# Kernel optimization log

Hardware: AMD Instinct MI355X
Metric: run time of the kernel (lower is better)

## Reference

```python
import jax, jax.numpy as jnp
import numpy as np

LAYERS = 2          # init kwarg 'layers'
DEPTH = 4           # init kwarg 'depth' (StronglyEntanglingLayers depth)
N_QUBITS = 4
MULT = float(np.pi - np.finfo(np.float32).eps)


def _apply_1q(state, U, q):
    """state: (B,2,2,2,2) complex; U: (2,2) or (B,2,2) complex; wire q (axis 1+q, MSB-first)."""
    st = jnp.moveaxis(state, 1 + q, -1)
    if U.ndim == 3:
        st = jnp.einsum('bij,b...j->b...i', U, st)
    else:
        st = jnp.einsum('ij,...j->...i', U, st)
    return jnp.moveaxis(st, -1, 1 + q)


def _apply_cnot(state, c, t):
    st = jnp.moveaxis(state, (1 + c, 1 + t), (-2, -1))
    st = jnp.stack([st[..., 0, :], st[..., 1, ::-1]], axis=-2)
    return jnp.moveaxis(st, (-2, -1), (1 + c, 1 + t))


def _ry(theta):
    """RY(theta) -> (...,2,2) complex64; theta may be batched."""
    c = jnp.cos(theta / 2).astype(jnp.complex64)
    s = jnp.sin(theta / 2).astype(jnp.complex64)
    return jnp.stack([jnp.stack([c, -s], -1), jnp.stack([s, c], -1)], -2)


def _rot(phi, theta, omega):
    """qml.Rot = RZ(omega) RY(theta) RZ(phi), scalar params -> (2,2) complex64."""
    c = jnp.cos(theta / 2)
    s = jnp.sin(theta / 2)
    ep = jnp.exp(-0.5j * (phi + omega).astype(jnp.complex64))
    em = jnp.exp(0.5j * (phi - omega).astype(jnp.complex64))
    row0 = jnp.stack([ep * c, -em * s])
    row1 = jnp.stack([jnp.conj(em) * s, jnp.conj(ep) * c])
    return jnp.stack([row0, row1])


def _circuit(x, w, n_out):
    """AngleEmbedding(Y) + StronglyEntanglingLayers on 4 qubits.
    x: (B,4) angles; w: (L,4,3); returns (B, n_out) PauliZ expvals."""
    B = x.shape[0]
    state = jnp.zeros((B, 16), jnp.complex64).at[:, 0].set(1.0).reshape(B, 2, 2, 2, 2)
    for q in range(N_QUBITS):
        state = _apply_1q(state, _ry(x[:, q]), q)  # batched RY embedding
    L = w.shape[0]
    for l in range(L):
        for q in range(N_QUBITS):
            state = _apply_1q(state, _rot(w[l, q, 0], w[l, q, 1], w[l, q, 2]), q)
        r = (l % (N_QUBITS - 1)) + 1  # default SEL ranges: 1,2,3,1,...
        for q in range(N_QUBITS):
            state = _apply_cnot(state, q, (q + r) % N_QUBITS)
    probs = state.real ** 2 + state.imag ** 2  # (B,2,2,2,2)
    outs = []
    for q in range(n_out):
        axes = tuple(a for a in range(1, 5) if a != 1 + q)
        pq = probs.sum(axes)  # (B,2)
        outs.append(pq[:, 0] - pq[:, 1])
    return jnp.stack(outs, axis=1)


def _forward(x_, theta):
    B = x_.shape[0]
    z = jnp.zeros((B, 1), x_.dtype)
    H = jnp.concatenate([z, x_, z, z], axis=1)  # (B,16)
    c44 = jax.vmap(lambda xb, wb: _circuit(xb, wb, 4))  # over 4 blocks
    c41 = jax.vmap(lambda xb, wb: _circuit(xb, wb, 1))
    # layer 0: 'first' -> contiguous 4-wide blocks
    blocks = H.reshape(B, 4, 4).transpose(1, 0, 2)  # (block, B, 4)
    H = c44(blocks, theta[0]).transpose(1, 0, 2).reshape(B, 16)
    # hidden layers: 'multiple' -> block j = column j of each old block
    for i in range(LAYERS):
        blocks = H.reshape(B, 4, 4).transpose(2, 0, 1)  # (j, B, old_block)
        H = c44(blocks, theta[i + 3]).transpose(1, 0, 2).reshape(B, 16)
    # 16 -> 4 : 'multiple' transpose, 4to1 readout per block
    blocks = H.reshape(B, 4, 4).transpose(2, 0, 1)
    H = c41(blocks, theta[1]).transpose(1, 0, 2).reshape(B, 4)
    # 4 -> 1 : single block, only theta[2][0] is used (matches original loop)
    H = _circuit(H, theta[2, 0], 1)  # (B,1)
    return (H * MULT).astype(jnp.float32)


def setup_inputs() -> dict:
    key = jax.random.key(0)
    k1, k2 = jax.random.split(key)
    x_ = jax.random.uniform(k1, (32768, 13), dtype=jnp.float32)
    theta = 0.01 * jax.random.normal(k2, (LAYERS + 3, 4, DEPTH, 4, 3), dtype=jnp.float32)
    return {"x_": x_, "theta": theta}


def reference(x_, theta):
    return _forward(x_, theta)
```

## Files before the change

kernel.cpp:

```cpp
#include <hip/hip_runtime.h>
#include <math.h>


typedef _Float16 half8 __attribute__((ext_vector_type(8)));
typedef float floatx16 __attribute__((ext_vector_type(16)));

#define N_CIRC 17
__device__ __constant__ constexpr int PERM[3][16] = {
  {0, 9, 11, 2, 15, 6, 4, 13, 7, 14, 12, 5, 8, 1, 3, 10},
  {0, 5, 10, 15, 1, 4, 11, 14, 2, 7, 8, 13, 3, 6, 9, 12},
  {0, 3, 6, 5, 12, 15, 10, 9, 11, 8, 13, 14, 7, 4, 1, 2},
};

__global__ void __launch_bounds__(64) build_M_kernel(
    const float* __restrict__ theta, _Float16* __restrict__ M) {
  int idx = blockIdx.x * 64 + threadIdx.x;
  if (idx >= N_CIRC * 16) return;
  int c = idx >> 4, j = idx & 15;
  int tt, blk;
  if (c < 4)       { tt = 0; blk = c; }
  else if (c < 8)  { tt = 3; blk = c - 4; }
  else if (c < 12) { tt = 4; blk = c - 8; }
  else if (c < 16) { tt = 1; blk = c - 12; }
  else             { tt = 2; blk = 0; }
  float sr[16], si[16];
#pragma unroll
  for (int i = 0; i < 16; ++i) { sr[i] = 0.f; si[i] = 0.f; }
  sr[j] = 1.f;
#pragma unroll
  for (int l = 0; l < 4; ++l) {
#pragma unroll
    for (int q = 0; q < 4; ++q) {
      const float* th = theta + (((tt * 4 + blk) * 16) + l * 4 + q) * 3;
      float phi = th[0], the = th[1], ome = th[2];
      float st, ct;   __sincosf(0.5f * the, &st, &ct);
      float sap, cap; __sincosf(0.5f * (phi + ome), &sap, &cap);
      float sam, cam; __sincosf(0.5f * (phi - ome), &sam, &cam);
      float u00r =  cap * ct, u00i = -sap * ct;
      float u01r = -cam * st, u01i = -sam * st;
      float u10r =  cam * st, u10i = -sam * st;
      float u11r =  cap * ct, u11i =  sap * ct;
      const int m = 8 >> q;
#pragma unroll
      for (int i = 0; i < 16; ++i) {
        if (i & m) continue;
        const int i1 = i | m;
        float ar = sr[i], ai = si[i], br = sr[i1], bi = si[i1];
        sr[i]  = u00r * ar - u00i * ai + u01r * br - u01i * bi;
        si[i]  = u00r * ai + u00i * ar + u01r * bi + u01i * br;
        sr[i1] = u10r * ar - u10i * ai + u11r * br - u11i * bi;
        si[i1] = u10r * ai + u10i * ar + u11r * bi + u11i * br;
      }
    }
    const int ri = (l == 3) ? 0 : l;
    float tr[16], ti[16];
#pragma unroll
    for (int i = 0; i < 16; ++i) { tr[i] = sr[i]; ti[i] = si[i]; }
#pragma unroll
    for (int i = 0; i < 16; ++i) { sr[PERM[ri][i]] = tr[i]; si[PERM[ri][i]] = ti[i]; }
  }
#pragma unroll
  for (int m = 0; m < 32; ++m) {
    float val = (m & 1) ? si[m >> 1] : sr[m >> 1];
    int lane = ((j >> 3) << 5) | m;
    M[(size_t)(c * 64 + lane) * 8 + (j & 7)] = (_Float16)val;
  }
}

__device__ __forceinline__ void run_circ(
    const _Float16* __restrict__ M, int ci, int lane, int g,
    float a0, float a1, float a2, float a3, bool full,
    float& o0, float& o1, float& o2, float& o3) {
  float s0, c0, s1, c1, s2, c2, s3, c3;
  __sincosf(0.5f * a0, &s0, &c0);
  __sincosf(0.5f * a1, &s1, &c1);
  __sincosf(0.5f * a2, &s2, &c2);
  __sincosf(0.5f * a3, &s3, &c3);
  float w0 = g ? s0 : c0;
  float u0 = w0 * c1, u1 = w0 * s1;
  float w23[4] = {c2 * c3, c2 * s3, s2 * c3, s2 * s3};
  half8 bf;
#pragma unroll
  for (int t = 0; t < 8; ++t)
    bf[t] = (_Float16)(((t < 4) ? u0 : u1) * w23[t & 3]);
  half8 a = *(const half8*)&M[(size_t)(ci * 64 + lane) * 8];
  floatx16 z = {0.f,0.f,0.f,0.f,0.f,0.f,0.f,0.f,
                0.f,0.f,0.f,0.f,0.f,0.f,0.f,0.f};
  floatx16 acc = __builtin_amdgcn_mfma_f32_32x32x16_f16(a, bf, z, 0, 0, 0);
  float p[4][2];
#pragma unroll
  for (int qq = 0; qq < 4; ++qq)
#pragma unroll
    for (int h = 0; h < 2; ++h)
      p[qq][h] = acc[4 * qq + 2 * h]     * acc[4 * qq + 2 * h]
               + acc[4 * qq + 2 * h + 1] * acc[4 * qq + 2 * h + 1];
  float S4[4], D4[4];
#pragma unroll
  for (int qq = 0; qq < 4; ++qq) {
    S4[qq] = p[qq][0] + p[qq][1];
    D4[qq] = p[qq][0] - p[qq][1];
  }
  o0 = (S4[0] + S4[1]) - (S4[2] + S4[3]);
  o0 += __shfl_xor(o0, 32);
  if (full) {
    o1 = (S4[0] - S4[1]) + (S4[2] - S4[3]);
    float S = (S4[0] + S4[1]) + (S4[2] + S4[3]);
    o2 = g ? -S : S;
    o3 = (D4[0] + D4[1]) + (D4[2] + D4[3]);
    o1 += __shfl_xor(o1, 32);
    o2 += __shfl_xor(o2, 32);
    o3 += __shfl_xor(o3, 32);
  }
}

__global__ void __launch_bounds__(64) vqc_reg_kernel(
    const float* __restrict__ x, const _Float16* __restrict__ M,
    float* __restrict__ out, int B) {
  const int lane = threadIdx.x;
  const int g = lane >> 5, n = lane & 31;
  const int row = blockIdx.x * 32 + n;

  float xv[13];
  const float* xp = x + (size_t)(row < B ? row : 0) * 13;
#pragma unroll
  for (int j = 0; j < 13; ++j) xv[j] = xp[j];

  float e[4][4];
  float d0 = 0.f, d1 = 0.f, d2 = 0.f;

  run_circ(M, 0, lane, g, 0.f,    xv[0],  xv[1],  xv[2],  true,
           e[0][0], e[0][1], e[0][2], e[0][3]);
  run_circ(M, 1, lane, g, xv[3],  xv[4],  xv[5],  xv[6],  true,
           e[1][0], e[1][1], e[1][2], e[1][3]);
  run_circ(M, 2, lane, g, xv[7],  xv[8],  xv[9],  xv[10], true,
           e[2][0], e[2][1], e[2][2], e[2][3]);
  run_circ(M, 3, lane, g, xv[11], xv[12], 0.f,    0.f,    true,
           e[3][0], e[3][1], e[3][2], e[3][3]);

#pragma unroll
  for (int s = 1; s <= 2; ++s) {
    float ne[4][4];
#pragma unroll
    for (int w = 0; w < 4; ++w)
      run_circ(M, s * 4 + w, lane, g, e[0][w], e[1][w], e[2][w], e[3][w],
               true, ne[w][0], ne[w][1], ne[w][2], ne[w][3]);
#pragma unroll
    for (int w = 0; w < 4; ++w)
#pragma unroll
      for (int j = 0; j < 4; ++j) e[w][j] = ne[w][j];
  }

  float f[4];
#pragma unroll
  for (int w = 0; w < 4; ++w)
    run_circ(M, 12 + w, lane, g, e[0][w], e[1][w], e[2][w], e[3][w],
             false, f[w], d0, d1, d2);

  float r;
  run_circ(M, 16, lane, g, f[0], f[1], f[2], f[3], false, r, d0, d1, d2);

  if (g == 0 && row < B) {
    const float MULT = (float)(3.141592653589793 - 1.1920928955078125e-07);
    out[row] = r * MULT;
  }
}

extern "C" void kernel_launch(void* const* d_in, const int* in_sizes, int n_in,
                              void* d_out, int out_size, void* d_ws, size_t ws_size,
                              hipStream_t stream) {
  const float* x     = (const float*)d_in[0];
  const float* theta = (const float*)d_in[1];
  float* out = (float*)d_out;
  _Float16* M = (_Float16*)d_ws;
  int B = in_sizes[0] / 13;
  hipLaunchKernelGGL(build_M_kernel, dim3((N_CIRC * 16 + 63) / 64), dim3(64),
                     0, stream, theta, M);
  int blocks = (B + 31) / 32;
  hipLaunchKernelGGL(vqc_reg_kernel, dim3(blocks), dim3(64), 0, stream,
                     x, M, out, B);
}
```

Before: 64.94 us.

## Parallelize circuit matrix build across lanes with shuffles instead of per-thread statevectors

```diff
diff --git a/kernel.cpp b/kernel.cpp
--- a/kernel.cpp
+++ b/kernel.cpp
@@ -6,27 +6,29 @@
 typedef float floatx16 __attribute__((ext_vector_type(16)));
 
 #define N_CIRC 17
-__device__ __constant__ constexpr int PERM[3][16] = {
-  {0, 9, 11, 2, 15, 6, 4, 13, 7, 14, 12, 5, 8, 1, 3, 10},
-  {0, 5, 10, 15, 1, 4, 11, 14, 2, 7, 8, 13, 3, 6, 9, 12},
-  {0, 3, 6, 5, 12, 15, 10, 9, 11, 8, 13, 14, 7, 4, 1, 2},
+__device__ __constant__ constexpr int PERM_INV[3][16] = {
+  {0, 13, 3, 14, 6, 11, 5, 8, 12, 1, 15, 2, 10, 7, 9, 4},
+  {0, 4, 8, 12, 5, 1, 13, 9, 10, 14, 2, 6, 15, 11, 7, 3},
+  {0, 14, 15, 1, 13, 3, 2, 12, 9, 7, 6, 8, 4, 10, 11, 5},
 };
 
-__global__ void __launch_bounds__(64) build_M_kernel(
+__global__ void __launch_bounds__(256) build_M_kernel(
     const float* __restrict__ theta, _Float16* __restrict__ M) {
-  int idx = blockIdx.x * 64 + threadIdx.x;
-  if (idx >= N_CIRC * 16) return;
-  int c = idx >> 4, j = idx & 15;
+  const int c   = blockIdx.x;
+  const int tid = threadIdx.x;
+  const int j   = tid >> 4;
+  const int i   = tid & 15;
+  const int lane = tid & 63;
   int tt, blk;
   if (c < 4)       { tt = 0; blk = c; }
   else if (c < 8)  { tt = 3; blk = c - 4; }
   else if (c < 12) { tt = 4; blk = c - 8; }
   else if (c < 16) { tt = 1; blk = c - 12; }
   else             { tt = 2; blk = 0; }
-  float sr[16], si[16];
-#pragma unroll
-  for (int i = 0; i < 16; ++i) { sr[i] = 0.f; si[i] = 0.f; }
-  sr[j] = 1.f;
+
+  float sr = (i == j) ? 1.f : 0.f;
+  float si = 0.f;
+
 #pragma unroll
   for (int l = 0; l < 4; ++l) {
 #pragma unroll
@@ -41,30 +43,23 @@
       float u10r =  cam * st, u10i = -sam * st;
       float u11r =  cap * ct, u11i =  sap * ct;
       const int m = 8 >> q;
-#pragma unroll
-      for (int i = 0; i < 16; ++i) {
-        if (i & m) continue;
-        const int i1 = i | m;
-        float ar = sr[i], ai = si[i], br = sr[i1], bi = si[i1];
-        sr[i]  = u00r * ar - u00i * ai + u01r * br - u01i * bi;
-        si[i]  = u00r * ai + u00i * ar + u01r * bi + u01i * br;
-        sr[i1] = u10r * ar - u10i * ai + u11r * br - u11i * bi;
-        si[i1] = u10r * ai + u10i * ar + u11r * bi + u11i * br;
-      }
+      float pr = __shfl_xor(sr, m);
+      float pi = __shfl_xor(si, m);
+      const bool hi = (i & m) != 0;
+      float car = hi ? u11r : u00r, cai = hi ? u11i : u00i;
+      float cbr = hi ? u10r : u01r, cbi = hi ? u10i : u01i;
+      float nsr = car * sr - cai * si + cbr * pr - cbi * pi;
+      float nsi = car * si + cai * sr + cbr * pi + cbi * pr;
+      sr = nsr; si = nsi;
     }
     const int ri = (l == 3) ? 0 : l;
-    float tr[16], ti[16];
-#pragma unroll
-    for (int i = 0; i < 16; ++i) { tr[i] = sr[i]; ti[i] = si[i]; }
-#pragma unroll
-    for (int i = 0; i < 16; ++i) { sr[PERM[ri][i]] = tr[i]; si[PERM[ri][i]] = ti[i]; }
+    const int src = (lane & ~15) | PERM_INV[ri][i];
+    sr = __shfl(sr, src);
+    si = __shfl(si, src);
   }
-#pragma unroll
-  for (int m = 0; m < 32; ++m) {
-    float val = (m & 1) ? si[m >> 1] : sr[m >> 1];
-    int lane = ((j >> 3) << 5) | m;
-    M[(size_t)(c * 64 + lane) * 8 + (j & 7)] = (_Float16)val;
-  }
+  const int ln0 = ((j >> 3) << 5) | (2 * i);
+  M[(size_t)(c * 64 + ln0) * 8 + (j & 7)]       = (_Float16)sr;
+  M[(size_t)(c * 64 + (ln0 | 1)) * 8 + (j & 7)] = (_Float16)si;
 }
 
 __device__ __forceinline__ void run_circ(
@@ -173,8 +168,8 @@
   float* out = (float*)d_out;
   _Float16* M = (_Float16*)d_ws;
   int B = in_sizes[0] / 13;
-  hipLaunchKernelGGL(build_M_kernel, dim3((N_CIRC * 16 + 63) / 64), dim3(64),
-                     0, stream, theta, M);
+  hipLaunchKernelGGL(build_M_kernel, dim3(N_CIRC), dim3(256), 0, stream,
+                     theta, M);
   int blocks = (B + 31) / 32;
   hipLaunchKernelGGL(vqc_reg_kernel, dim3(blocks), dim3(64), 0, stream,
                      x, M, out, B);
```

Measured after the change: 61.93 us. -4.6%, faster.
